# Kernel optimization log

Measured on AMD Instinct MI355X. Metric: run time of the kernel, lower is better.

Reference implementation:

```python
import jax, jax.numpy as jnp
import numpy as np

D_MODEL = 1024
HEADS = 16
D_FF = 4096
EPS = 1e-6
NEG = -1e9


def setup_inputs() -> dict:
    key = jax.random.key(0)
    ks = jax.random.split(key, 12)
    B, S, D = 2, 2048, D_MODEL
    s = 0.02
    return {
        "x": jax.random.normal(ks[0], (B, S, D), dtype=jnp.float32),
        "mask": jax.random.randint(ks[1], (B, 1, S), 0, 2, dtype=jnp.int32),
        "alpha1": jnp.ones((D,), jnp.float32),
        "bias1": jnp.zeros((D,), jnp.float32),
        "alpha2": jnp.ones((D,), jnp.float32),
        "bias2": jnp.zeros((D,), jnp.float32),
        "Wk": jax.random.normal(ks[2], (D, D), jnp.float32) * s,
        "bk": jnp.zeros((D,), jnp.float32),
        "Wv": jax.random.normal(ks[3], (D, D), jnp.float32) * s,
        "bv": jnp.zeros((D,), jnp.float32),
        "Wo": jax.random.normal(ks[4], (D, D), jnp.float32) * s,
        "bo": jnp.zeros((D,), jnp.float32),
        "W1": jax.random.normal(ks[5], (D, D_FF), jnp.float32) * s,
        "b1": jnp.zeros((D_FF,), jnp.float32),
        "W2": jax.random.normal(ks[6], (D_FF, D), jnp.float32) * s,
        "b2": jnp.zeros((D,), jnp.float32),
    }


def _norm(x, alpha, bias):
    # torch Norm: unbiased std (ddof=1), eps added to std (not variance)
    mu = jnp.mean(x, axis=-1, keepdims=True)
    sd = jnp.std(x, axis=-1, keepdims=True, ddof=1)
    return alpha * (x - mu) / (sd + EPS) + bias


def reference(x, mask, alpha1, bias1, alpha2, bias2,
              Wk, bk, Wv, bv, Wo, bo, W1, b1, W2, b2):
    B, S, D = x.shape
    H, dk = HEADS, D // HEADS

    x2 = _norm(x, alpha1, bias1)
    # NOTE: source bug preserved: q uses k_linear weights
    q = (x2 @ Wk + bk).reshape(B, S, H, dk).transpose(0, 2, 1, 3)  # [B,H,S,dk]
    k = (x2 @ Wk + bk).reshape(B, S, H, dk).transpose(0, 2, 1, 3)
    v = (x2 @ Wv + bv).reshape(B, S, H, dk).transpose(0, 2, 1, 3)

    scores = jnp.einsum('bhqd,bhkd->bhqk', q, k) / jnp.sqrt(jnp.float32(dk))
    scores = jnp.where(mask[:, None, :, :] == 0, NEG, scores)  # [B,1,1,S] broadcast
    attn = jax.nn.softmax(scores, axis=-1)
    ctx = jnp.einsum('bhqk,bhkd->bhqd', attn, v)
    concat = ctx.transpose(0, 2, 1, 3).reshape(B, S, D)
    x = x + (concat @ Wo + bo)

    x2 = _norm(x, alpha2, bias2)
    ff = jax.nn.relu(x2 @ W1 + b1) @ W2 + b2
    return x + ff
```

## Files before the change

kernel.cpp:

```cpp
#include <hip/hip_runtime.h>
#include <hip/hip_bf16.h>
#include <math.h>

typedef __bf16 bf16_t;
typedef __bf16 bf16x8 __attribute__((ext_vector_type(8)));
typedef __bf16 bf16x4 __attribute__((ext_vector_type(4)));
typedef float  f32x4  __attribute__((ext_vector_type(4)));

#define MFMA16(a,b,c) __builtin_amdgcn_mfma_f32_16x16x32_bf16((a),(b),(c),0,0,0)

__device__ static inline void gload_lds16(const void* g, void* l) {
    __builtin_amdgcn_global_load_lds((const __attribute__((address_space(1))) void*)g,
                                     (__attribute__((address_space(3))) void*)l, 16, 0, 0);
}

__device__ static inline float exp2_hw(float x) {
#if __has_builtin(__builtin_amdgcn_exp2f)
    return __builtin_amdgcn_exp2f(x);
#else
    float r; asm("v_exp_f32 %0, %1" : "=v"(r) : "v"(x)); return r;
#endif
}

__device__ static inline float max3f(float a, float b, float c) {
    return fmaxf(fmaxf(a, b), c);
}

__global__ __launch_bounds__(256)
void transpose_f2b(const float* __restrict__ in, bf16_t* __restrict__ out, int R, int C)
{
    __shared__ float t[32][33];
    const int tx = threadIdx.x & 31, ty = threadIdx.x >> 5;
    const int r0 = blockIdx.y << 5, c0 = blockIdx.x << 5;
#pragma unroll
    for (int i = 0; i < 4; ++i)
        t[ty + i*8][tx] = in[(size_t)(r0 + ty + i*8) * C + c0 + tx];
    __syncthreads();
#pragma unroll
    for (int i = 0; i < 4; ++i)
        out[(size_t)(c0 + ty + i*8) * R + r0 + tx] = (bf16_t)t[tx][ty + i*8];
}

__global__ __launch_bounds__(256)
void transpose_b2b(const bf16_t* __restrict__ in, bf16_t* __restrict__ out, int R, int C, int ldi)
{
    __shared__ bf16_t t[32][33];
    const int tx = threadIdx.x & 31, ty = threadIdx.x >> 5;
    const int r0 = blockIdx.y << 5, c0 = blockIdx.x << 5;
#pragma unroll
    for (int i = 0; i < 4; ++i)
        t[ty + i*8][tx] = in[(size_t)(r0 + ty + i*8) * ldi + c0 + tx];
    __syncthreads();
#pragma unroll
    for (int i = 0; i < 4; ++i)
        out[(size_t)(c0 + ty + i*8) * R + r0 + tx] = t[tx][ty + i*8];
}

__global__ __launch_bounds__(256)
void concat_bias(const float* __restrict__ a, const float* __restrict__ b, float* __restrict__ o)
{
    const int i = blockIdx.x * 256 + threadIdx.x;
    o[i] = (i < 1024) ? a[i] : b[i - 1024];
}

__global__ __launch_bounds__(256)
void mask_bias_k(const int* __restrict__ mask, float* __restrict__ mb)
{
    const int i = blockIdx.x * 256 + threadIdx.x;
    mb[i] = (mask[i] == 0) ? -16384.0f : 0.0f;
}

__global__ __launch_bounds__(256)
void layernorm_k(const float* __restrict__ x, const float* __restrict__ gam,
                 const float* __restrict__ bet, bf16_t* __restrict__ out)
{
    const int row = blockIdx.x, tid = threadIdx.x;
    const float4 v = ((const float4*)(x + (size_t)row * 1024))[tid];
    float s  = v.x + v.y + v.z + v.w;
    float ss = v.x*v.x + v.y*v.y + v.z*v.z + v.w*v.w;
#pragma unroll
    for (int off = 32; off >= 1; off >>= 1) {
        s  += __shfl_xor(s,  off);
        ss += __shfl_xor(ss, off);
    }
    __shared__ float rs[4], rq[4];
    if ((tid & 63) == 0) { rs[tid >> 6] = s; rq[tid >> 6] = ss; }
    __syncthreads();
    s  = rs[0] + rs[1] + rs[2] + rs[3];
    ss = rq[0] + rq[1] + rq[2] + rq[3];
    const float mu  = s * (1.0f / 1024.0f);
    const float var = fmaxf((ss - 1024.0f * mu * mu) * (1.0f / 1023.0f), 0.0f);
    const float inv = 1.0f / (sqrtf(var) + 1e-6f);
    const int c = tid << 2;
    bf16x4 o;
    o[0] = (bf16_t)(gam[c+0] * ((v.x - mu) * inv) + bet[c+0]);
    o[1] = (bf16_t)(gam[c+1] * ((v.y - mu) * inv) + bet[c+1]);
    o[2] = (bf16_t)(gam[c+2] * ((v.z - mu) * inv) + bet[c+2]);
    o[3] = (bf16_t)(gam[c+3] * ((v.w - mu) * inv) + bet[c+3]);
    *(bf16x4*)(out + (size_t)row * 1024 + c) = o;
}

template<bool RELU, bool RES, int NFR, bool DBUF>
__global__ __launch_bounds__(256, 2)
void gemm128(const bf16_t* __restrict__ A, const bf16_t* __restrict__ Bt,
             const float* __restrict__ bias, const float* __restrict__ res,
             bf16_t* __restrict__ Cb, float* __restrict__ Cf,
             int M, int N, int K)
{
    constexpr int NTILE = NFR * 32;
    constexpr int NBUF = DBUF ? 2 : 1;
    __shared__ __align__(16) bf16_t As[NBUF][128 * 64];
    __shared__ __align__(16) bf16_t Bs[NBUF][NTILE * 64];
    const int tid  = threadIdx.x;
    const int lane = tid & 63;
    const int wid  = tid >> 6;
    const int wr = wid >> 1, wc = wid & 1;
    const int ntn = N / NTILE;
    const int cpx = gridDim.x >> 3;
    const int swz = (blockIdx.x & 7) * cpx + (blockIdx.x >> 3);
    const int bm = (swz / ntn) << 7;
    const int bn = (swz % ntn) * NTILE;
    const int l15 = lane & 15;
    const int g   = lane >> 4;

    f32x4 acc[4][NFR];
#pragma unroll
    for (int i = 0; i < 4; ++i)
#pragma unroll
        for (int j = 0; j < NFR; ++j)
#pragma unroll
            for (int e = 0; e < 4; ++e) acc[i][j][e] = 0.0f;

    const int srow = tid >> 3;
    const int scb  = (((tid & 7) << 4) ^ ((srow & 7) << 4));
    const bf16_t* Ab = A  + (size_t)(bm + srow) * K + (scb >> 1);
    const bf16_t* Bb = Bt + (size_t)(bn + srow) * K + (scb >> 1);

    auto stage = [&](int buf, int kt) {
        const int k0 = kt << 6;
        bf16_t* AsB = As[buf] + wid * 512;
        bf16_t* BsB = Bs[buf] + wid * 512;
#pragma unroll
        for (int it = 0; it < 4; ++it)
            gload_lds16(Ab + k0 + (size_t)(it * 32) * K, AsB + it * 2048);
#pragma unroll
        for (int it = 0; it < NFR; ++it)
            gload_lds16(Bb + k0 + (size_t)(it * 32) * K, BsB + it * 2048);
    };

    auto compute = [&](int buf) {
        bf16x8 af[4][2], bfr[NFR][2];
#pragma unroll
        for (int mi = 0; mi < 4; ++mi) {
            const int ar = (wr << 6) + mi * 16 + l15;
#pragma unroll
            for (int ks = 0; ks < 2; ++ks) {
                const int kb = (ks << 6) + (g << 4);
                af[mi][ks] = *(const bf16x8*)((const char*)As[buf] + ar * 128 + (kb ^ ((ar & 7) << 4)));
            }
        }
#pragma unroll
        for (int ni = 0; ni < NFR; ++ni) {
            const int br = wc * (NFR * 16) + ni * 16 + l15;
#pragma unroll
            for (int ks = 0; ks < 2; ++ks) {
                const int kb = (ks << 6) + (g << 4);
                bfr[ni][ks] = *(const bf16x8*)((const char*)Bs[buf] + br * 128 + (kb ^ ((br & 7) << 4)));
            }
        }
#pragma unroll
        for (int mi = 0; mi < 4; ++mi)
#pragma unroll
            for (int ni = 0; ni < NFR; ++ni) {
                acc[mi][ni] = MFMA16(af[mi][0], bfr[ni][0], acc[mi][ni]);
                acc[mi][ni] = MFMA16(af[mi][1], bfr[ni][1], acc[mi][ni]);
            }
    };

    const int nK = K >> 6;
    if constexpr (DBUF) {
        stage(0, 0);
        __syncthreads();
        for (int kt = 0; kt < nK; ++kt) {
            const int cur = kt & 1;
            if (kt + 1 < nK) stage(cur ^ 1, kt + 1);
            compute(cur);
            __syncthreads();
        }
    } else {
        for (int kt = 0; kt < nK; ++kt) {
            stage(0, kt);
            __syncthreads();
            compute(0);
            __syncthreads();
        }
    }

#pragma unroll
    for (int mi = 0; mi < 4; ++mi)
#pragma unroll
        for (int ni = 0; ni < NFR; ++ni) {
            const int gc = bn + wc * (NFR * 16) + ni * 16 + l15;
            const float bv = bias[gc];
#pragma unroll
            for (int j = 0; j < 4; ++j) {
                const int gr = bm + (wr << 6) + mi * 16 + (g << 2) + j;
                float vv = acc[mi][ni][j] + bv;
                if (RELU) vv = fmaxf(vv, 0.0f);
                if (RES)  Cf[(size_t)gr * N + gc] = vv + res[(size_t)gr * N + gc];
                else      Cb[(size_t)gr * N + gc] = (bf16_t)vv;
            }
        }
}

__global__ __launch_bounds__(256, 3)
void attn_kernel(const bf16_t* __restrict__ qkv, const bf16_t* __restrict__ vT,
                 const float* __restrict__ mbias, bf16_t* __restrict__ ctx)
{
    __shared__ __align__(16) bf16_t Ks[2][64 * 64];
    __shared__ __align__(16) bf16_t Vs[2][64 * 64];
    __shared__ __align__(16) char   Ps[4][4096];

    const int tid = threadIdx.x, lane = tid & 63, wid = tid >> 6;
    const int l15 = lane & 15, g = lane >> 4;
    const int id = blockIdx.x;
    const int qt = (id >> 3) & 15;
    const int bh = (id & 7) * 4 + (id >> 7);
    const int b = bh >> 4, h = bh & 15;
    const size_t rowQ = (size_t)(b * 2048 + qt * 128 + wid * 32);
    const float C = 0.18033688f;

    bf16x8 qf[2][2];
#pragma unroll
    for (int qfi = 0; qfi < 2; ++qfi)
#pragma unroll
        for (int ks = 0; ks < 2; ++ks)
            qf[qfi][ks] = *(const bf16x8*)(qkv + (rowQ + qfi*16 + l15) * 2048
                                           + h*64 + ks*32 + g*8);

    bf16x8 vones;
#pragma unroll
    for (int e = 0; e < 8; ++e) vones[e] = (bf16_t)1.0f;

    f32x4 O[2][4], l_acc[2];
#pragma unroll
    for (int mf = 0; mf < 2; ++mf) {
#pragma unroll
        for (int df = 0; df < 4; ++df)
#pragma unroll
            for (int e = 0; e < 4; ++e) O[mf][df][e] = 0.0f;
#pragma unroll
        for (int e = 0; e < 4; ++e) l_acc[mf][e] = 0.0f;
    }
    float m_t[2] = {0.0f, 0.0f};

    const int srow = tid >> 3;
    const int scb  = (((tid & 7) << 4) ^ ((srow & 7) << 4));
    const bf16_t* Kb = qkv + (size_t)(b*2048 + srow) * 2048 + h*64 + (scb >> 1);
    const bf16_t* Vb = vT  + (size_t)(h*64 + srow) * 4096 + b*2048 + (scb >> 1);
    const float*  Mb = mbias + b*2048;
    bf16_t* Ks0 = Ks[0] + wid * 512;  bf16_t* Ks1 = Ks[1] + wid * 512;
    bf16_t* Vs0 = Vs[0] + wid * 512;  bf16_t* Vs1 = Vs[1] + wid * 512;

    #define STAGE(KD, VD, KT)                                        \
        do {                                                         \
            gload_lds16(Kb + (size_t)(KT) * 2048, (KD));             \
            gload_lds16(Kb + (size_t)((KT) + 32) * 2048, (KD) + 2048);\
            gload_lds16(Vb + (KT), (VD));                            \
            gload_lds16(Vb + (size_t)32 * 4096 + (KT), (VD) + 2048); \
        } while (0)

    STAGE(Ks0, Vs0, 0);
    __syncthreads();

    char* Pw = Ps[wid];

    for (int kt_i = 0; kt_i < 32; ++kt_i) {
        const int kt = kt_i << 6;
        const bool cur1 = (kt_i & 1);
        if (kt_i < 31) {
            if (cur1) STAGE(Ks0, Vs0, kt + 64);
            else      STAGE(Ks1, Vs1, kt + 64);
        }
        const char* Kc = (const char*)(cur1 ? Ks[1] : Ks[0]);
        const char* Vc = (const char*)(cur1 ? Vs[1] : Vs[0]);

        bf16x8 kf[4][2];
#pragma unroll
        for (int kfi = 0; kfi < 4; ++kfi) {
            const int kr = kfi*16 + l15;
#pragma unroll
            for (int ks = 0; ks < 2; ++ks)
                kf[kfi][ks] = *(const bf16x8*)(Kc + kr*128
                                               + ((ks*64 + g*16) ^ ((kr & 7) << 4)));
        }
        f32x4 st[4][2];
#pragma unroll
        for (int kfi = 0; kfi < 4; ++kfi)
#pragma unroll
            for (int qfi = 0; qfi < 2; ++qfi) {
                f32x4 t;
#pragma unroll
                for (int e = 0; e < 4; ++e) t[e] = 0.0f;
                t = MFMA16(kf[kfi][0], qf[qfi][0], t);
                t = MFMA16(kf[kfi][1], qf[qfi][1], t);
                st[kfi][qfi] = t;
            }

        bf16x8 vf[4][2];
#pragma unroll
        for (int df = 0; df < 4; ++df) {
            const int vr = df*16 + l15;
#pragma unroll
            for (int ks = 0; ks < 2; ++ks)
                vf[df][ks] = *(const bf16x8*)(Vc + vr*128
                                              + ((ks*64 + g*16) ^ ((vr & 7) << 4)));
        }

#pragma unroll
        for (int kfi = 0; kfi < 4; ++kfi) {
            const float4 bb = *(const float4*)(Mb + kt + kfi*16 + g*4);
            const float* bj = (const float*)&bb;
#pragma unroll
            for (int j = 0; j < 4; ++j)
#pragma unroll
                for (int qfi = 0; qfi < 2; ++qfi)
                    st[kfi][qfi][j] = fmaf(st[kfi][qfi][j], C, bj[j]);
        }
        float mx[2];
#pragma unroll
        for (int qfi = 0; qfi < 2; ++qfi) {
            const float t0 = max3f(st[0][qfi][0], st[0][qfi][1], st[0][qfi][2]);
            const float t1 = max3f(st[0][qfi][3], st[1][qfi][0], st[1][qfi][1]);
            const float t2 = max3f(st[1][qfi][2], st[1][qfi][3], st[2][qfi][0]);
            const float t3 = max3f(st[2][qfi][1], st[2][qfi][2], st[2][qfi][3]);
            const float t4 = max3f(st[3][qfi][0], st[3][qfi][1], st[3][qfi][2]);
            float mxq = fmaxf(max3f(t0, t1, t2), max3f(t3, t4, st[3][qfi][3]));
            mxq = fmaxf(mxq, __shfl_xor(mxq, 16));
            mxq = fmaxf(mxq, __shfl_xor(mxq, 32));
            mx[qfi] = mxq;
        }
        if (__any((mx[0] > m_t[0] + 8.0f) || (mx[1] > m_t[1] + 8.0f))) {
            float cr[2];
#pragma unroll
            for (int qfi = 0; qfi < 2; ++qfi) {
                const float mn = fmaxf(m_t[qfi], mx[qfi]);
                cr[qfi] = exp2_hw(m_t[qfi] - mn);
                m_t[qfi] = mn;
            }
#pragma unroll
            for (int mf = 0; mf < 2; ++mf)
#pragma unroll
                for (int j = 0; j < 4; ++j) {
                    const float cj = __shfl(cr[mf], g*4 + j);
#pragma unroll
                    for (int df = 0; df < 4; ++df) O[mf][df][j] *= cj;
                    l_acc[mf][j] *= cj;
                }
        }
#pragma unroll
        for (int qfi = 0; qfi < 2; ++qfi) {
            const int q = qfi*16 + l15;
#pragma unroll
            for (int kfi = 0; kfi < 4; ++kfi) {
                bf16x4 pk;
#pragma unroll
                for (int j = 0; j < 4; ++j)
                    pk[j] = (bf16_t)exp2_hw(st[kfi][qfi][j] - m_t[qfi]);
                *(bf16x4*)(Pw + q*128 + ((kfi*32 + g*8) ^ ((l15 & 7) << 4))) = pk;
            }
        }
        bf16x8 pa[2][2];
#pragma unroll
        for (int mf = 0; mf < 2; ++mf) {
            const int r = mf*16 + l15;
#pragma unroll
            for (int ks = 0; ks < 2; ++ks)
                pa[mf][ks] = *(const bf16x8*)(Pw + r*128 + ((ks*64 + g*16) ^ ((l15 & 7) << 4)));
        }
#pragma unroll
        for (int mf = 0; mf < 2; ++mf) {
#pragma unroll
            for (int df = 0; df < 4; ++df) {
                O[mf][df] = MFMA16(pa[mf][0], vf[df][0], O[mf][df]);
                O[mf][df] = MFMA16(pa[mf][1], vf[df][1], O[mf][df]);
            }
            l_acc[mf] = MFMA16(pa[mf][0], vones, l_acc[mf]);
            l_acc[mf] = MFMA16(pa[mf][1], vones, l_acc[mf]);
        }
        __syncthreads();
    }
    #undef STAGE

#pragma unroll
    for (int mf = 0; mf < 2; ++mf)
#pragma unroll
        for (int j = 0; j < 4; ++j) {
            const float ri = __builtin_amdgcn_rcpf(l_acc[mf][j]);
            const size_t gr = rowQ + mf*16 + g*4 + j;
#pragma unroll
            for (int df = 0; df < 4; ++df)
                ctx[gr * 1024 + h*64 + df*16 + l15] = (bf16_t)(O[mf][df][j] * ri);
        }
}

extern "C" void kernel_launch(void* const* d_in, const int* in_sizes, int n_in,
                              void* d_out, int out_size, void* d_ws, size_t ws_size,
                              hipStream_t stream)
{
    const float* x   = (const float*)d_in[0];
    const int*   msk = (const int*)  d_in[1];
    const float* a1  = (const float*)d_in[2];
    const float* be1 = (const float*)d_in[3];
    const float* a2  = (const float*)d_in[4];
    const float* be2 = (const float*)d_in[5];
    const float* Wk  = (const float*)d_in[6];
    const float* bk  = (const float*)d_in[7];
    const float* Wv  = (const float*)d_in[8];
    const float* bv  = (const float*)d_in[9];
    const float* Wo  = (const float*)d_in[10];
    const float* bo  = (const float*)d_in[11];
    const float* W1  = (const float*)d_in[12];
    const float* b1  = (const float*)d_in[13];
    const float* W2  = (const float*)d_in[14];
    const float* b2  = (const float*)d_in[15];
    float* out = (float*)d_out;

    char* ws = (char*)d_ws;
    const size_t MB = 1u << 20;
    if (ws_size < 78 * MB) return;
    bf16_t* WkT = (bf16_t*)(ws + 0 * MB);
    bf16_t* WvT = (bf16_t*)(ws + 2 * MB);
    bf16_t* WoT = (bf16_t*)(ws + 4 * MB);
    bf16_t* W1T = (bf16_t*)(ws + 6 * MB);
    bf16_t* W2T = (bf16_t*)(ws + 14 * MB);
    bf16_t* x2  = (bf16_t*)(ws + 22 * MB);
    bf16_t* qkv = (bf16_t*)(ws + 30 * MB);
    bf16_t* vTb = (bf16_t*)(ws + 46 * MB);
    bf16_t* ctx = (bf16_t*)(ws + 54 * MB);
    float*  xn  = (float*) (ws + 62 * MB);
    float*  bkv   = (float*)(ws + 62 * MB);
    float*  mbias = (float*)(ws + 62 * MB + 32768);
    bf16_t* hb  = (bf16_t*)(ws + 30 * MB);

    dim3 blk(256);
    transpose_f2b<<<dim3(32, 32),  blk, 0, stream>>>(Wk, WkT, 1024, 1024);
    transpose_f2b<<<dim3(32, 32),  blk, 0, stream>>>(Wv, WvT, 1024, 1024);
    transpose_f2b<<<dim3(32, 32),  blk, 0, stream>>>(Wo, WoT, 1024, 1024);
    transpose_f2b<<<dim3(128, 32), blk, 0, stream>>>(W1, W1T, 1024, 4096);
    transpose_f2b<<<dim3(32, 128), blk, 0, stream>>>(W2, W2T, 4096, 1024);
    concat_bias<<<8, blk, 0, stream>>>(bk, bv, bkv);
    mask_bias_k<<<16, blk, 0, stream>>>(msk, mbias);

    layernorm_k<<<4096, blk, 0, stream>>>(x, a1, be1, x2);
    gemm128<false,false,4,true><<<dim3(32 * 16), blk, 0, stream>>>(x2, WkT, bkv, nullptr, qkv, nullptr, 4096, 2048, 1024);
    transpose_b2b<<<dim3(32, 128), blk, 0, stream>>>(qkv + 1024, vTb, 4096, 1024, 2048);
    attn_kernel<<<dim3(512), blk, 0, stream>>>(qkv, vTb, mbias, ctx);
    gemm128<false,true,2,true><<<dim3(32 * 16), blk, 0, stream>>>(ctx, WoT, bo, x,  nullptr, xn, 4096, 1024, 1024);
    layernorm_k<<<4096, blk, 0, stream>>>(xn, a2, be2, x2);
    gemm128<true,false,4,false><<<dim3(32 * 32), blk, 0, stream>>>(x2, W1T, b1, nullptr, hb, nullptr, 4096, 4096, 1024);
    gemm128<false,true,2,true><<<dim3(32 * 16), blk, 0, stream>>>(hb, W2T, b2, xn, nullptr, out, 4096, 1024, 4096);
}
```

Before: 242.2 us.

## Split attention key tile across waves and apply mask via zeroed V and flag rowsum

```diff
diff --git a/kernel.cpp b/kernel.cpp
--- a/kernel.cpp
+++ b/kernel.cpp
@@ -42,7 +42,8 @@
 }
 
 __global__ __launch_bounds__(256)
-void transpose_b2b(const bf16_t* __restrict__ in, bf16_t* __restrict__ out, int R, int C, int ldi)
+void transpose_b2b_mask(const bf16_t* __restrict__ in, bf16_t* __restrict__ out,
+                        const int* __restrict__ mask, int R, int C, int ldi)
 {
     __shared__ bf16_t t[32][33];
     const int tx = threadIdx.x & 31, ty = threadIdx.x >> 5;
@@ -51,9 +52,10 @@
     for (int i = 0; i < 4; ++i)
         t[ty + i*8][tx] = in[(size_t)(r0 + ty + i*8) * ldi + c0 + tx];
     __syncthreads();
+    const bool live = (mask[r0 + tx] != 0);
 #pragma unroll
     for (int i = 0; i < 4; ++i)
-        out[(size_t)(c0 + ty + i*8) * R + r0 + tx] = t[tx][ty + i*8];
+        out[(size_t)(c0 + ty + i*8) * R + r0 + tx] = live ? t[tx][ty + i*8] : (bf16_t)0.0f;
 }
 
 __global__ __launch_bounds__(256)
@@ -64,10 +66,10 @@
 }
 
 __global__ __launch_bounds__(256)
-void mask_bias_k(const int* __restrict__ mask, float* __restrict__ mb)
+void mask_flag_k(const int* __restrict__ mask, bf16_t* __restrict__ mf)
 {
     const int i = blockIdx.x * 256 + threadIdx.x;
-    mb[i] = (mask[i] == 0) ? -16384.0f : 0.0f;
+    mf[i] = (mask[i] == 0) ? (bf16_t)0.0f : (bf16_t)1.0f;
 }
 
 __global__ __launch_bounds__(256)
@@ -213,22 +215,24 @@
         }
 }
 
-__global__ __launch_bounds__(256, 3)
+__global__ __launch_bounds__(256, 4)
 void attn_kernel(const bf16_t* __restrict__ qkv, const bf16_t* __restrict__ vT,
-                 const float* __restrict__ mbias, bf16_t* __restrict__ ctx)
+                 const bf16_t* __restrict__ flags, bf16_t* __restrict__ ctx)
 {
     __shared__ __align__(16) bf16_t Ks[2][64 * 64];
     __shared__ __align__(16) bf16_t Vs[2][64 * 64];
-    __shared__ __align__(16) char   Ps[4][4096];
+    __shared__ __align__(16) char   Ps[8192];
 
     const int tid = threadIdx.x, lane = tid & 63, wid = tid >> 6;
     const int l15 = lane & 15, g = lane >> 4;
+    const int qw = wid & 1, kw = wid >> 1;
     const int id = blockIdx.x;
-    const int qt = (id >> 3) & 15;
-    const int bh = (id & 7) * 4 + (id >> 7);
+    const int qt = (id >> 3) & 31;
+    const int bh = (id & 7) * 4 + (id >> 8);
     const int b = bh >> 4, h = bh & 15;
-    const size_t rowQ = (size_t)(b * 2048 + qt * 128 + wid * 32);
+    const size_t rowQ = (size_t)(b * 2048 + qt * 64 + qw * 32);
     const float C = 0.18033688f;
+    const float THR = 44.0f;
 
     bf16x8 qf[2][2];
 #pragma unroll
@@ -237,10 +241,6 @@
         for (int ks = 0; ks < 2; ++ks)
             qf[qfi][ks] = *(const bf16x8*)(qkv + (rowQ + qfi*16 + l15) * 2048
                                            + h*64 + ks*32 + g*8);
-
-    bf16x8 vones;
-#pragma unroll
-    for (int e = 0; e < 8; ++e) vones[e] = (bf16_t)1.0f;
 
     f32x4 O[2][4], l_acc[2];
 #pragma unroll
@@ -258,7 +258,7 @@
     const int scb  = (((tid & 7) << 4) ^ ((srow & 7) << 4));
     const bf16_t* Kb = qkv + (size_t)(b*2048 + srow) * 2048 + h*64 + (scb >> 1);
     const bf16_t* Vb = vT  + (size_t)(h*64 + srow) * 4096 + b*2048 + (scb >> 1);
-    const float*  Mb = mbias + b*2048;
+    const bf16_t* Fb = flags + b*2048;
     bf16_t* Ks0 = Ks[0] + wid * 512;  bf16_t* Ks1 = Ks[1] + wid * 512;
     bf16_t* Vs0 = Vs[0] + wid * 512;  bf16_t* Vs1 = Vs[1] + wid * 512;
 
@@ -273,7 +273,7 @@
     STAGE(Ks0, Vs0, 0);
     __syncthreads();
 
-    char* Pw = Ps[wid];
+    char* Pw = Ps + qw * 4096 + kw * 2048;
 
     for (int kt_i = 0; kt_i < 32; ++kt_i) {
         const int kt = kt_i << 6;
@@ -285,18 +285,19 @@
         const char* Kc = (const char*)(cur1 ? Ks[1] : Ks[0]);
         const char* Vc = (const char*)(cur1 ? Vs[1] : Vs[0]);
 
-        bf16x8 kf[4][2];
-#pragma unroll
-        for (int kfi = 0; kfi < 4; ++kfi) {
-            const int kr = kfi*16 + l15;
+        bf16x8 kf[2][2];
+#pragma unroll
+        for (int kfi = 0; kfi < 2; ++kfi) {
+            const int kr = kw*32 + kfi*16 + l15;
 #pragma unroll
             for (int ks = 0; ks < 2; ++ks)
                 kf[kfi][ks] = *(const bf16x8*)(Kc + kr*128
                                                + ((ks*64 + g*16) ^ ((kr & 7) << 4)));
         }
-        f32x4 st[4][2];
-#pragma unroll
-        for (int kfi = 0; kfi < 4; ++kfi)
+        f32x4 st[2][2];
+        __builtin_amdgcn_s_setprio(1);
+#pragma unroll
+        for (int kfi = 0; kfi < 2; ++kfi)
 #pragma unroll
             for (int qfi = 0; qfi < 2; ++qfi) {
                 f32x4 t;
@@ -306,46 +307,25 @@
                 t = MFMA16(kf[kfi][1], qf[qfi][1], t);
                 st[kfi][qfi] = t;
             }
-
-        bf16x8 vf[4][2];
-#pragma unroll
-        for (int df = 0; df < 4; ++df) {
-            const int vr = df*16 + l15;
-#pragma unroll
-            for (int ks = 0; ks < 2; ++ks)
-                vf[df][ks] = *(const bf16x8*)(Vc + vr*128
-                                              + ((ks*64 + g*16) ^ ((vr & 7) << 4)));
-        }
-
-#pragma unroll
-        for (int kfi = 0; kfi < 4; ++kfi) {
-            const float4 bb = *(const float4*)(Mb + kt + kfi*16 + g*4);
-            const float* bj = (const float*)&bb;
-#pragma unroll
-            for (int j = 0; j < 4; ++j)
-#pragma unroll
-                for (int qfi = 0; qfi < 2; ++qfi)
-                    st[kfi][qfi][j] = fmaf(st[kfi][qfi][j], C, bj[j]);
-        }
+        __builtin_amdgcn_s_setprio(0);
+
         float mx[2];
 #pragma unroll
         for (int qfi = 0; qfi < 2; ++qfi) {
             const float t0 = max3f(st[0][qfi][0], st[0][qfi][1], st[0][qfi][2]);
             const float t1 = max3f(st[0][qfi][3], st[1][qfi][0], st[1][qfi][1]);
-            const float t2 = max3f(st[1][qfi][2], st[1][qfi][3], st[2][qfi][0]);
-            const float t3 = max3f(st[2][qfi][1], st[2][qfi][2], st[2][qfi][3]);
-            const float t4 = max3f(st[3][qfi][0], st[3][qfi][1], st[3][qfi][2]);
-            float mxq = fmaxf(max3f(t0, t1, t2), max3f(t3, t4, st[3][qfi][3]));
+            const float t2 = max3f(st[1][qfi][2], st[1][qfi][3], t0);
+            float mxq = max3f(t1, t2, st[0][qfi][0]);
             mxq = fmaxf(mxq, __shfl_xor(mxq, 16));
             mxq = fmaxf(mxq, __shfl_xor(mxq, 32));
             mx[qfi] = mxq;
         }
-        if (__any((mx[0] > m_t[0] + 8.0f) || (mx[1] > m_t[1] + 8.0f))) {
+        if (__any((mx[0] > m_t[0] + THR) || (mx[1] > m_t[1] + THR))) {
             float cr[2];
 #pragma unroll
             for (int qfi = 0; qfi < 2; ++qfi) {
                 const float mn = fmaxf(m_t[qfi], mx[qfi]);
-                cr[qfi] = exp2_hw(m_t[qfi] - mn);
+                cr[qfi] = exp2_hw((m_t[qfi] - mn) * C);
                 m_t[qfi] = mn;
             }
 #pragma unroll
@@ -358,50 +338,101 @@
                     l_acc[mf][j] *= cj;
                 }
         }
+        const float nmC0 = -m_t[0] * C, nmC1 = -m_t[1] * C;
 #pragma unroll
         for (int qfi = 0; qfi < 2; ++qfi) {
+            const float nm = qfi ? nmC1 : nmC0;
             const int q = qfi*16 + l15;
 #pragma unroll
-            for (int kfi = 0; kfi < 4; ++kfi) {
+            for (int kfi = 0; kfi < 2; ++kfi) {
                 bf16x4 pk;
 #pragma unroll
                 for (int j = 0; j < 4; ++j)
-                    pk[j] = (bf16_t)exp2_hw(st[kfi][qfi][j] - m_t[qfi]);
-                *(bf16x4*)(Pw + q*128 + ((kfi*32 + g*8) ^ ((l15 & 7) << 4))) = pk;
-            }
-        }
-        bf16x8 pa[2][2];
+                    pk[j] = (bf16_t)exp2_hw(fmaf(st[kfi][qfi][j], C, nm));
+                *(bf16x4*)(Pw + q*64 + ((kfi*32 + g*8) ^ ((q & 3) << 4))) = pk;
+            }
+        }
+        const bf16x8 ff = *(const bf16x8*)(Fb + kt + kw*32 + g*8);
+        bf16x8 pa[2], vf[4];
 #pragma unroll
         for (int mf = 0; mf < 2; ++mf) {
-            const int r = mf*16 + l15;
-#pragma unroll
-            for (int ks = 0; ks < 2; ++ks)
-                pa[mf][ks] = *(const bf16x8*)(Pw + r*128 + ((ks*64 + g*16) ^ ((l15 & 7) << 4)));
-        }
+            const int q = mf*16 + l15;
+            pa[mf] = *(const bf16x8*)(Pw + q*64 + ((g*16) ^ ((q & 3) << 4)));
+        }
+#pragma unroll
+        for (int df = 0; df < 4; ++df) {
+            const int vr = df*16 + l15;
+            vf[df] = *(const bf16x8*)(Vc + vr*128 + ((kw*64 + g*16) ^ ((vr & 7) << 4)));
+        }
+        __builtin_amdgcn_s_setprio(1);
 #pragma unroll
         for (int mf = 0; mf < 2; ++mf) {
 #pragma unroll
-            for (int df = 0; df < 4; ++df) {
-                O[mf][df] = MFMA16(pa[mf][0], vf[df][0], O[mf][df]);
-                O[mf][df] = MFMA16(pa[mf][1], vf[df][1], O[mf][df]);
-            }
-            l_acc[mf] = MFMA16(pa[mf][0], vones, l_acc[mf]);
-            l_acc[mf] = MFMA16(pa[mf][1], vones, l_acc[mf]);
-        }
+            for (int df = 0; df < 4; ++df)
+                O[mf][df] = MFMA16(pa[mf], vf[df], O[mf][df]);
+            l_acc[mf] = MFMA16(pa[mf], ff, l_acc[mf]);
+        }
+        __builtin_amdgcn_s_setprio(0);
         __syncthreads();
     }
     #undef STAGE
 
-#pragma unroll
-    for (int mf = 0; mf < 2; ++mf)
-#pragma unroll
-        for (int j = 0; j < 4; ++j) {
-            const float ri = __builtin_amdgcn_rcpf(l_acc[mf][j]);
-            const size_t gr = rowQ + mf*16 + g*4 + j;
+    float* Pf = (float*)(Ps) + qw * 1024;
+    if (kw == 1) {
+        if (l15 == 0) {
+#pragma unroll
+            for (int mf = 0; mf < 2; ++mf)
+#pragma unroll
+                for (int j = 0; j < 4; ++j)
+                    Pf[mf*16 + g*4 + j] = l_acc[mf][j];
+        }
+        if (lane == 0) { Pf[32] = m_t[0]; Pf[33] = m_t[1]; }
+    }
+    __syncthreads();
+    float wa[2] = {1.0f, 1.0f}, wb[2] = {0.0f, 0.0f};
+    f32x4 l_new[2];
+#pragma unroll
+    for (int mf = 0; mf < 2; ++mf) {
+        const float mb_ = Pf[32 + mf];
+        const float ms = fmaxf(m_t[mf], mb_);
+        wa[mf] = exp2_hw((m_t[mf] - ms) * C);
+        wb[mf] = exp2_hw((mb_ - ms) * C);
+#pragma unroll
+        for (int j = 0; j < 4; ++j)
+            l_new[mf][j] = l_acc[mf][j] * wa[mf] + Pf[mf*16 + g*4 + j] * wb[mf];
+    }
+    __syncthreads();
+#pragma unroll
+    for (int mf = 0; mf < 2; ++mf) {
+        if (kw == 1) {
 #pragma unroll
             for (int df = 0; df < 4; ++df)
-                ctx[gr * 1024 + h*64 + df*16 + l15] = (bf16_t)(O[mf][df][j] * ri);
-        }
+#pragma unroll
+                for (int j = 0; j < 4; ++j)
+                    Pf[lane*16 + df*4 + j] = O[mf][df][j];
+        }
+        __syncthreads();
+        if (kw == 0) {
+#pragma unroll
+            for (int df = 0; df < 4; ++df)
+#pragma unroll
+                for (int j = 0; j < 4; ++j)
+                    O[mf][df][j] = O[mf][df][j] * wa[mf] + Pf[lane*16 + df*4 + j] * wb[mf];
+        }
+        __syncthreads();
+    }
+    if (kw == 0) {
+#pragma unroll
+        for (int mf = 0; mf < 2; ++mf)
+#pragma unroll
+            for (int j = 0; j < 4; ++j) {
+                const float ri = __builtin_amdgcn_rcpf(l_new[mf][j]);
+                const size_t gr = rowQ + mf*16 + g*4 + j;
+#pragma unroll
+                for (int df = 0; df < 4; ++df)
+                    ctx[gr * 1024 + h*64 + df*16 + l15] = (bf16_t)(O[mf][df][j] * ri);
+            }
+    }
 }
 
 extern "C" void kernel_launch(void* const* d_in, const int* in_sizes, int n_in,
@@ -440,7 +471,7 @@
     bf16_t* ctx = (bf16_t*)(ws + 54 * MB);
     float*  xn  = (float*) (ws + 62 * MB);
     float*  bkv   = (float*)(ws + 62 * MB);
-    float*  mbias = (float*)(ws + 62 * MB + 32768);
+    bf16_t* mflag = (bf16_t*)(ws + 62 * MB + 32768);
     bf16_t* hb  = (bf16_t*)(ws + 30 * MB);
 
     dim3 blk(256);
@@ -450,12 +481,12 @@
     transpose_f2b<<<dim3(128, 32), blk, 0, stream>>>(W1, W1T, 1024, 4096);
     transpose_f2b<<<dim3(32, 128), blk, 0, stream>>>(W2, W2T, 4096, 1024);
     concat_bias<<<8, blk, 0, stream>>>(bk, bv, bkv);
-    mask_bias_k<<<16, blk, 0, stream>>>(msk, mbias);
+    mask_flag_k<<<16, blk, 0, stream>>>(msk, mflag);
 
     layernorm_k<<<4096, blk, 0, stream>>>(x, a1, be1, x2);
     gemm128<false,false,4,true><<<dim3(32 * 16), blk, 0, stream>>>(x2, WkT, bkv, nullptr, qkv, nullptr, 4096, 2048, 1024);
-    transpose_b2b<<<dim3(32, 128), blk, 0, stream>>>(qkv + 1024, vTb, 4096, 1024, 2048);
-    attn_kernel<<<dim3(512), blk, 0, stream>>>(qkv, vTb, mbias, ctx);
+    transpose_b2b_mask<<<dim3(32, 128), blk, 0, stream>>>(qkv + 1024, vTb, msk, 4096, 1024, 2048);
+    attn_kernel<<<dim3(1024), blk, 0, stream>>>(qkv, vTb, mflag, ctx);
     gemm128<false,true,2,true><<<dim3(32 * 16), blk, 0, stream>>>(ctx, WoT, bo, x,  nullptr, xn, 4096, 1024, 1024);
     layernorm_k<<<4096, blk, 0, stream>>>(xn, a2, be2, x2);
     gemm128<true,false,4,false><<<dim3(32 * 32), blk, 0, stream>>>(x2, W1T, b1, nullptr, hb, nullptr, 4096, 4096, 1024);
```

Measured after the change: 254.4 us. 1.05x slower.
